# Optimization experiments

Measured on AMD Instinct MI355X. Metric: run time of the kernel, lower is better.

Reference implementation:

```python
import jax, jax.numpy as jnp
import numpy as np

H = 128  # rnn_features


def setup_inputs() -> dict:
    key = jax.random.key(0)
    ks = jax.random.split(key, 9)
    B, T, D = 1024, 256, 128
    x = jax.random.normal(ks[0], (B, T, D), dtype=jnp.float32)
    hidden_state = jax.random.normal(ks[1], (1, B, H), dtype=jnp.float32)
    done = jax.random.randint(ks[2], (B, T), 0, 2, dtype=jnp.int32)
    s = 1.0 / np.sqrt(H)
    W_ih = jax.random.uniform(ks[3], (3 * H, D), jnp.float32, -s, s)
    W_hh = jax.random.uniform(ks[4], (3 * H, H), jnp.float32, -s, s)
    b_ih = jax.random.uniform(ks[5], (3 * H,), jnp.float32, -s, s)
    b_hh = jax.random.uniform(ks[6], (3 * H,), jnp.float32, -s, s)
    fc_W = jax.random.uniform(ks[7], (H, H), jnp.float32, -s, s)
    fc_b = jax.random.uniform(ks[8], (H,), jnp.float32, -s, s)
    return {"x": x, "hidden_state": hidden_state, "done": done,
            "W_ih": W_ih, "W_hh": W_hh, "b_ih": b_ih, "b_hh": b_hh,
            "fc_W": fc_W, "fc_b": fc_b}


def _gru_with_resets(x, h0, done, W_ih, W_hh, b_ih, b_hh):
    # x: [B,T,D], h0: [B,H], done: [B,T] int
    B, T, D = x.shape
    # reset multiplier applied BEFORE step t: 1 - done[:, t-1]; no reset at t=0
    done_f = done.astype(x.dtype)
    reset = 1.0 - jnp.concatenate([jnp.zeros((B, 1), x.dtype), done_f[:, :-1]], axis=1)  # [B,T]
    # precompute input projections in one big GEMM: [B,T,3H]
    xi = jnp.einsum('btd,gd->btg', x, W_ih) + b_ih
    xi_T = jnp.transpose(xi, (1, 0, 2))      # [T,B,3H]
    reset_T = jnp.transpose(reset, (1, 0))   # [T,B]

    def step(h, inp):
        xi_t, r_t = inp
        h = h * r_t[:, None]
        gh = h @ W_hh.T + b_hh               # [B,3H]
        r = jax.nn.sigmoid(xi_t[:, :H] + gh[:, :H])
        z = jax.nn.sigmoid(xi_t[:, H:2 * H] + gh[:, H:2 * H])
        n = jnp.tanh(xi_t[:, 2 * H:] + r * gh[:, 2 * H:])
        h = (1.0 - z) * n + z * h
        return h, h

    h_last, hs = jax.lax.scan(step, h0, (xi_T, reset_T))
    return jnp.transpose(hs, (1, 0, 2)), h_last  # [B,T,H], [B,H]


def reference(x, hidden_state, done, W_ih, W_hh, b_ih, b_hh, fc_W, fc_b):
    # body_net is identity; fcs = Linear + ELU
    rfeat, h_last = _gru_with_resets(x, hidden_state[0], done, W_ih, W_hh, b_ih, b_hh)
    out = jax.nn.elu(jnp.einsum('bth,oh->bto', rfeat, fc_W) + fc_b)
    return out, h_last[None]  # hidden back to [1,B,H]
```

## Files before the change

kernel.cpp:

```cpp
#include <hip/hip_runtime.h>
#include <hip/hip_bf16.h>
#include <math.h>

#define Hd 128
#define Tt 256
#define Bb 1024
#define CL 32
#define NCK (Tt / CL)

typedef __attribute__((ext_vector_type(8))) short short8;
typedef __attribute__((ext_vector_type(4))) float f32x4;

__device__ __forceinline__ short f2bf(float f) {
    unsigned u = __float_as_uint(f);
    u += 0x7fffu + ((u >> 16) & 1u);
    return (short)(u >> 16);
}
__device__ __forceinline__ float bflo(unsigned u) { return __uint_as_float(u << 16); }
__device__ __forceinline__ float bfhi(unsigned u) { return __uint_as_float(u & 0xffff0000u); }

__global__ void prep_weights(const float* __restrict__ Wih,
                             const float* __restrict__ Whh,
                             const float* __restrict__ fcW,
                             short* __restrict__ oIh, short* __restrict__ oHh,
                             short* __restrict__ oFc) {
    int t = blockIdx.x * 256 + threadIdx.x;
    if (t >= 14336) return;
    const float* src;
    short* dst;
    if (t < 6144)       { src = Wih; dst = oIh + t * 8; }
    else if (t < 12288) { t -= 6144;  src = Whh; dst = oHh + t * 8; }
    else                { t -= 12288; src = fcW; dst = oFc + t * 8; }
    int lane = t & 63, kf = (t >> 6) & 3, nt = t >> 8;
    const float* s = src + (nt * 16 + (lane & 15)) * 128 + kf * 32 + 8 * (lane >> 4);
#pragma unroll
    for (int j = 0; j < 8; j++) dst[j] = f2bf(s[j]);
}

__global__ __launch_bounds__(512)
void xi_gemm(const float* __restrict__ x, const float* __restrict__ bih,
             const float* __restrict__ bhh, const short* __restrict__ wIh,
             short* __restrict__ xi_l) {
    __shared__ short xs[64 * 136];
    const int tid = threadIdx.x, wv = tid >> 6, ln = tid & 63;
    const int q = ln & 15, lg = ln >> 4;
    const int bg = blockIdx.x;
    const int sl0 = blockIdx.y * 4;
    {
        const int row = tid >> 3, kq = tid & 7;
        const int b = row & 15, dt = row >> 4;
        const float* xp = x + (((size_t)(bg * 16 + b)) * Tt + (sl0 + dt)) * Hd + kq * 16;
        f32x4 u0 = *(const f32x4*)&xp[0],  u1 = *(const f32x4*)&xp[4];
        f32x4 u2 = *(const f32x4*)&xp[8],  u3 = *(const f32x4*)&xp[12];
        short8 s0, s1;
#pragma unroll
        for (int i = 0; i < 4; i++) { s0[i] = f2bf(u0[i]); s0[i+4] = f2bf(u1[i]);
                                      s1[i] = f2bf(u2[i]); s1[i+4] = f2bf(u3[i]); }
        *(short8*)&xs[row * 136 + kq * 16] = s0;
        *(short8*)&xs[row * 136 + kq * 16 + 8] = s1;
    }
    __syncthreads();
    short8 wb[3][4];
#pragma unroll
    for (int i = 0; i < 3; i++)
#pragma unroll
        for (int kf = 0; kf < 4; kf++)
            wb[i][kf] = *(const short8*)&wIh[(((wv + 8 * i) * 4 + kf) * 64 + ln) * 8];
    float biasv[3];
#pragma unroll
    for (int i = 0; i < 3; i++) {
        int c = (wv + 8 * i) * 16 + q;
        biasv[i] = bih[c] + (c < 256 ? bhh[c] : 0.f);
    }
#pragma unroll 1
    for (int mt = 0; mt < 4; mt++) {
        short8 af[4];
#pragma unroll
        for (int kf = 0; kf < 4; kf++)
            af[kf] = *(const short8*)&xs[(mt * 16 + q) * 136 + kf * 32 + 8 * lg];
        f32x4 c0 = {0,0,0,0}, c1 = {0,0,0,0}, c2 = {0,0,0,0};
#pragma unroll
        for (int kf = 0; kf < 4; kf++) {
            c0 = __builtin_amdgcn_mfma_f32_16x16x32_bf16(af[kf], wb[0][kf], c0, 0, 0, 0);
            c1 = __builtin_amdgcn_mfma_f32_16x16x32_bf16(af[kf], wb[1][kf], c1, 0, 0, 0);
            c2 = __builtin_amdgcn_mfma_f32_16x16x32_bf16(af[kf], wb[2][kf], c2, 0, 0, 0);
        }
#pragma unroll
        for (int i = 0; i < 3; i++) {
            f32x4 cc = (i == 0) ? c0 : (i == 1) ? c1 : c2;
            unsigned d0 = (unsigned)(unsigned short)f2bf(cc[0] + biasv[i]) |
                          ((unsigned)(unsigned short)f2bf(cc[1] + biasv[i]) << 16);
            unsigned d1 = (unsigned)(unsigned short)f2bf(cc[2] + biasv[i]) |
                          ((unsigned)(unsigned short)f2bf(cc[3] + biasv[i]) << 16);
            uint2 dd = {d0, d1};
            ((uint2*)xi_l)[(((size_t)bg * Tt + (sl0 + mt)) * 24 + (wv + 8 * i)) * 64 + ln] = dd;
        }
    }
}

__global__ __launch_bounds__(256)
void gru_chunk(const short* __restrict__ xi_l, const int* __restrict__ done,
               const float* __restrict__ h0,
               const float* __restrict__ bhh, const float* __restrict__ fcb,
               const short* __restrict__ wHh, const short* __restrict__ wFc,
               float* __restrict__ out, float* __restrict__ hlast) {
    __shared__ short hT[2][16 * 136];
    __shared__ int doneL[Tt * 16];
    __shared__ int rbL[16];
    const int tid = threadIdx.x, j = tid >> 6, ln = tid & 63;
    const int q = ln & 15, lg = ln >> 4;
    const int bg = blockIdx.x, ck = blockIdx.y;
    const int t_c = ck * CL, t_end = t_c + CL;

    {
        const int b = tid >> 4, i = tid & 15;
        const int* dp = done + (size_t)(bg * 16 + b) * Tt;
        for (int t = i; t < t_end; t += 16) doneL[t * 16 + b] = dp[t];
    }
    __syncthreads();
    if (tid < 16) {
        int r = 0;
        for (int t = t_c - 1; t >= 0; --t)
            if (doneL[t * 16 + tid]) { r = t + 1; break; }
        rbL[tid] = r;
    }
    __syncthreads();
    int rmin = rbL[0];
#pragma unroll
    for (int b = 1; b < 16; b++) rmin = min(rmin, rbL[b]);

    short8 whh[6][4], wfc[2][4];
#pragma unroll
    for (int i = 0; i < 6; i++)
#pragma unroll
        for (int kf = 0; kf < 4; kf++)
            whh[i][kf] = *(const short8*)&wHh[(((j + 4 * i) * 4 + kf) * 64 + ln) * 8];
#pragma unroll
    for (int cs = 0; cs < 2; cs++)
#pragma unroll
        for (int kf = 0; kf < 4; kf++)
            wfc[cs][kf] = *(const short8*)&wFc[(((j + 4 * cs) * 4 + kf) * 64 + ln) * 8];
    float cbn[2], cbf[2];
#pragma unroll
    for (int cs = 0; cs < 2; cs++) {
        int c = 16 * j + 64 * cs + q;
        cbn[cs] = bhh[256 + c];
        cbf[cs] = fcb[c];
    }

    float h_reg[2][4];
#pragma unroll
    for (int cs = 0; cs < 2; cs++)
#pragma unroll
        for (int r = 0; r < 4; r++) {
            int bb = 4 * lg + r, c = 16 * j + 64 * cs + q;
            h_reg[cs][r] = (rbL[bb] == 0) ? h0[(size_t)(bg * 16 + bb) * Hd + c] : 0.f;
        }
    {
        int row = tid >> 4, c0 = (tid & 15) * 8;
        short8 s0 = {0,0,0,0,0,0,0,0};
        if (rbL[row] == 0) {
            const float* hp = &h0[(size_t)(bg * 16 + row) * Hd + c0];
            f32x4 u0 = *(const f32x4*)&hp[0], u1 = *(const f32x4*)&hp[4];
#pragma unroll
            for (int i = 0; i < 4; i++) { s0[i] = f2bf(u0[i]); s0[i+4] = f2bf(u1[i]); }
        }
        *(short8*)&hT[rmin & 1][row * 136 + c0] = s0;
    }
    __syncthreads();

    const uint2* xp = (const uint2*)xi_l + ((size_t)bg * Tt + rmin) * 1536 + j * 64 + ln;
    uint2 cur[6];
#pragma unroll
    for (int i = 0; i < 6; i++) cur[i] = xp[i * 256];
    xp += 1536;

#pragma unroll 1
    for (int t = rmin; t < t_end; ++t) {
        const short* hTp = &hT[t & 1][0];
        short* hTn = &hT[(t + 1) & 1][0];
        short8 haf[4];
#pragma unroll
        for (int kf = 0; kf < 4; kf++)
            haf[kf] = *(const short8*)&hTp[q * 136 + kf * 32 + 8 * lg];

        f32x4 acc[6];
#pragma unroll
        for (int i = 0; i < 4; i++) {
            f32x4 a = {bflo(cur[i].x), bfhi(cur[i].x), bflo(cur[i].y), bfhi(cur[i].y)};
            acc[i] = a;
        }
        { f32x4 a = {cbn[0], cbn[0], cbn[0], cbn[0]}; acc[4] = a; }
        { f32x4 a = {cbn[1], cbn[1], cbn[1], cbn[1]}; acc[5] = a; }
        uint2 xn8[2] = {cur[4], cur[5]};
        if (t + 1 < t_end) {
#pragma unroll
            for (int i = 0; i < 6; i++) cur[i] = xp[i * 256];
        }
        xp += 1536;

        if (t > t_c) {
            f32x4 fca[2];
            { f32x4 a = {cbf[0], cbf[0], cbf[0], cbf[0]}; fca[0] = a; }
            { f32x4 a = {cbf[1], cbf[1], cbf[1], cbf[1]}; fca[1] = a; }
#pragma unroll
            for (int kf = 0; kf < 4; kf++)
#pragma unroll
                for (int cs = 0; cs < 2; cs++)
                    fca[cs] = __builtin_amdgcn_mfma_f32_16x16x32_bf16(haf[kf], wfc[cs][kf], fca[cs], 0, 0, 0);
#pragma unroll
            for (int cs = 0; cs < 2; cs++)
#pragma unroll
                for (int r = 0; r < 4; r++) {
                    int bb = 4 * lg + r, c = 16 * j + 64 * cs + q;
                    float v = fca[cs][r];
                    float e = __expf(v) - 1.f;
                    v = v > 0.f ? v : e;
                    out[(((size_t)(bg * 16 + bb)) * Tt + (t - 1)) * Hd + c] = v;
                }
        }

        if (t > 0) {
            int dn = doneL[(t - 1) * 16 + q];
            short8 z8 = {0,0,0,0,0,0,0,0};
#pragma unroll
            for (int kf = 0; kf < 4; kf++) haf[kf] = dn ? z8 : haf[kf];
        }
        __builtin_amdgcn_s_setprio(1);
#pragma unroll
        for (int kf = 0; kf < 4; kf++)
#pragma unroll
            for (int i = 0; i < 6; i++)
                acc[i] = __builtin_amdgcn_mfma_f32_16x16x32_bf16(haf[kf], whh[i][kf], acc[i], 0, 0, 0);

        float rstf[4] = {1.f, 1.f, 1.f, 1.f};
        if (t > 0) {
            int4 dd = *(const int4*)&doneL[(t - 1) * 16 + 4 * lg];
            rstf[0] = dd.x ? 0.f : 1.f; rstf[1] = dd.y ? 0.f : 1.f;
            rstf[2] = dd.z ? 0.f : 1.f; rstf[3] = dd.w ? 0.f : 1.f;
        }
#pragma unroll
        for (int cs = 0; cs < 2; cs++) {
#pragma unroll
            for (int r = 0; r < 4; r++) {
                float rg = __builtin_amdgcn_rcpf(1.f + __expf(-acc[cs][r]));
                float zg = __builtin_amdgcn_rcpf(1.f + __expf(-acc[2 + cs][r]));
                float xn = (r == 0) ? bflo(xn8[cs].x) : (r == 1) ? bfhi(xn8[cs].x)
                         : (r == 2) ? bflo(xn8[cs].y) : bfhi(xn8[cs].y);
                float aa = fmaf(rg, acc[4 + cs][r], xn);
                float ng = 1.f - 2.f * __builtin_amdgcn_rcpf(__expf(2.f * aa) + 1.f);
                float hp = h_reg[cs][r] * rstf[r];
                float hn = (1.f - zg) * ng + zg * hp;
                h_reg[cs][r] = hn;
                hTn[(4 * lg + r) * 136 + 16 * j + 64 * cs + q] = f2bf(hn);
            }
        }
        __builtin_amdgcn_s_setprio(0);
        __builtin_amdgcn_sched_barrier(0);
        __builtin_amdgcn_s_waitcnt(0xC07F);
        __builtin_amdgcn_s_barrier();
        __builtin_amdgcn_sched_barrier(0);
    }
    {
        const short* hTp = &hT[t_end & 1][0];
        short8 haf[4];
#pragma unroll
        for (int kf = 0; kf < 4; kf++)
            haf[kf] = *(const short8*)&hTp[q * 136 + kf * 32 + 8 * lg];
        f32x4 fca[2];
        { f32x4 a = {cbf[0], cbf[0], cbf[0], cbf[0]}; fca[0] = a; }
        { f32x4 a = {cbf[1], cbf[1], cbf[1], cbf[1]}; fca[1] = a; }
#pragma unroll
        for (int kf = 0; kf < 4; kf++)
#pragma unroll
            for (int cs = 0; cs < 2; cs++)
                fca[cs] = __builtin_amdgcn_mfma_f32_16x16x32_bf16(haf[kf], wfc[cs][kf], fca[cs], 0, 0, 0);
#pragma unroll
        for (int cs = 0; cs < 2; cs++)
#pragma unroll
            for (int r = 0; r < 4; r++) {
                int bb = 4 * lg + r, c = 16 * j + 64 * cs + q;
                float v = fca[cs][r];
                float e = __expf(v) - 1.f;
                v = v > 0.f ? v : e;
                out[(((size_t)(bg * 16 + bb)) * Tt + (t_end - 1)) * Hd + c] = v;
            }
    }
    if (ck == NCK - 1) {
#pragma unroll
        for (int cs = 0; cs < 2; cs++)
#pragma unroll
            for (int r = 0; r < 4; r++) {
                int bb = 4 * lg + r, c = 16 * j + 64 * cs + q;
                hlast[(size_t)(bg * 16 + bb) * Hd + c] = h_reg[cs][r];
            }
    }
}

extern "C" void kernel_launch(void* const* d_in, const int* in_sizes, int n_in,
                              void* d_out, int out_size, void* d_ws, size_t ws_size,
                              hipStream_t stream) {
    const float* x   = (const float*)d_in[0];
    const float* h0  = (const float*)d_in[1];
    const int*   dn  = (const int*)d_in[2];
    const float* Wih = (const float*)d_in[3];
    const float* Whh = (const float*)d_in[4];
    const float* bih = (const float*)d_in[5];
    const float* bhh = (const float*)d_in[6];
    const float* fcW = (const float*)d_in[7];
    const float* fcb = (const float*)d_in[8];

    short* wIh = (short*)d_ws;
    short* wHh = wIh + 49152;
    short* wFc = wHh + 49152;
    short* xi_l = wFc + 16384;
    float* out = (float*)d_out;
    float* hlast = out + (size_t)Bb * Tt * Hd;

    prep_weights<<<56, 256, 0, stream>>>(Wih, Whh, fcW, wIh, wHh, wFc);
    xi_gemm<<<dim3(64, Tt / 4), 512, 0, stream>>>(x, bih, bhh, wIh, xi_l);
    gru_chunk<<<dim3(64, NCK), 256, 0, stream>>>(xi_l, dn, h0, bhh, fcb,
                                                 wHh, wFc, out, hlast);
}
```

Baseline: 164.8 us.

## Fuse input-projection GEMM into recurrent GRU kernel, dropping xi intermediate buffer

Removes the separate xi_gemm kernel and its bf16 xi intermediate buffer. The chunked GRU kernel now loads x rows per timestep, converts them to bf16 with packed cvt instructions, and computes the input projection with MFMAs inside the recurrence loop. The W_ih fragments are streamed from global/L2 each step instead of held in registers. This saves the intermediate write and read plus one launch, but adds MFMA work and weight loads to the serial per-step critical path. Chunks with a warm-up prefix also recompute the projection for the steps they replay.

```diff
diff --git a/kernel.cpp b/kernel.cpp
--- a/kernel.cpp
+++ b/kernel.cpp
@@ -16,8 +16,16 @@
     u += 0x7fffu + ((u >> 16) & 1u);
     return (short)(u >> 16);
 }
-__device__ __forceinline__ float bflo(unsigned u) { return __uint_as_float(u << 16); }
-__device__ __forceinline__ float bfhi(unsigned u) { return __uint_as_float(u & 0xffff0000u); }
+__device__ __forceinline__ f32x4 spl(float v) { f32x4 a = {v, v, v, v}; return a; }
+
+__device__ __forceinline__ short8 cvt8(f32x4 a, f32x4 b) {
+    union { unsigned u[4]; short8 s; } c;
+    asm("v_cvt_pk_bf16_f32 %0, %1, %2" : "=v"(c.u[0]) : "v"(a[0]), "v"(a[1]));
+    asm("v_cvt_pk_bf16_f32 %0, %1, %2" : "=v"(c.u[1]) : "v"(a[2]), "v"(a[3]));
+    asm("v_cvt_pk_bf16_f32 %0, %1, %2" : "=v"(c.u[2]) : "v"(b[0]), "v"(b[1]));
+    asm("v_cvt_pk_bf16_f32 %0, %1, %2" : "=v"(c.u[3]) : "v"(b[2]), "v"(b[3]));
+    return c.s;
+}
 
 __global__ void prep_weights(const float* __restrict__ Wih,
                              const float* __restrict__ Whh,
@@ -37,72 +45,21 @@
     for (int j = 0; j < 8; j++) dst[j] = f2bf(s[j]);
 }
 
-__global__ __launch_bounds__(512)
-void xi_gemm(const float* __restrict__ x, const float* __restrict__ bih,
-             const float* __restrict__ bhh, const short* __restrict__ wIh,
-             short* __restrict__ xi_l) {
-    __shared__ short xs[64 * 136];
-    const int tid = threadIdx.x, wv = tid >> 6, ln = tid & 63;
-    const int q = ln & 15, lg = ln >> 4;
-    const int bg = blockIdx.x;
-    const int sl0 = blockIdx.y * 4;
-    {
-        const int row = tid >> 3, kq = tid & 7;
-        const int b = row & 15, dt = row >> 4;
-        const float* xp = x + (((size_t)(bg * 16 + b)) * Tt + (sl0 + dt)) * Hd + kq * 16;
-        f32x4 u0 = *(const f32x4*)&xp[0],  u1 = *(const f32x4*)&xp[4];
-        f32x4 u2 = *(const f32x4*)&xp[8],  u3 = *(const f32x4*)&xp[12];
-        short8 s0, s1;
-#pragma unroll
-        for (int i = 0; i < 4; i++) { s0[i] = f2bf(u0[i]); s0[i+4] = f2bf(u1[i]);
-                                      s1[i] = f2bf(u2[i]); s1[i+4] = f2bf(u3[i]); }
-        *(short8*)&xs[row * 136 + kq * 16] = s0;
-        *(short8*)&xs[row * 136 + kq * 16 + 8] = s1;
-    }
-    __syncthreads();
-    short8 wb[3][4];
-#pragma unroll
-    for (int i = 0; i < 3; i++)
-#pragma unroll
-        for (int kf = 0; kf < 4; kf++)
-            wb[i][kf] = *(const short8*)&wIh[(((wv + 8 * i) * 4 + kf) * 64 + ln) * 8];
-    float biasv[3];
-#pragma unroll
-    for (int i = 0; i < 3; i++) {
-        int c = (wv + 8 * i) * 16 + q;
-        biasv[i] = bih[c] + (c < 256 ? bhh[c] : 0.f);
-    }
-#pragma unroll 1
-    for (int mt = 0; mt < 4; mt++) {
-        short8 af[4];
-#pragma unroll
-        for (int kf = 0; kf < 4; kf++)
-            af[kf] = *(const short8*)&xs[(mt * 16 + q) * 136 + kf * 32 + 8 * lg];
-        f32x4 c0 = {0,0,0,0}, c1 = {0,0,0,0}, c2 = {0,0,0,0};
-#pragma unroll
-        for (int kf = 0; kf < 4; kf++) {
-            c0 = __builtin_amdgcn_mfma_f32_16x16x32_bf16(af[kf], wb[0][kf], c0, 0, 0, 0);
-            c1 = __builtin_amdgcn_mfma_f32_16x16x32_bf16(af[kf], wb[1][kf], c1, 0, 0, 0);
-            c2 = __builtin_amdgcn_mfma_f32_16x16x32_bf16(af[kf], wb[2][kf], c2, 0, 0, 0);
-        }
-#pragma unroll
-        for (int i = 0; i < 3; i++) {
-            f32x4 cc = (i == 0) ? c0 : (i == 1) ? c1 : c2;
-            unsigned d0 = (unsigned)(unsigned short)f2bf(cc[0] + biasv[i]) |
-                          ((unsigned)(unsigned short)f2bf(cc[1] + biasv[i]) << 16);
-            unsigned d1 = (unsigned)(unsigned short)f2bf(cc[2] + biasv[i]) |
-                          ((unsigned)(unsigned short)f2bf(cc[3] + biasv[i]) << 16);
-            uint2 dd = {d0, d1};
-            ((uint2*)xi_l)[(((size_t)bg * Tt + (sl0 + mt)) * 24 + (wv + 8 * i)) * 64 + ln] = dd;
-        }
-    }
-}
+#define LOADW(W, i_) { const short* wb_ = wIh + ((j + 4 * (i_)) * 2048 + ln * 8); \
+    W[0] = *(const short8*)(wb_);        W[1] = *(const short8*)(wb_ + 512);      \
+    W[2] = *(const short8*)(wb_ + 1024); W[3] = *(const short8*)(wb_ + 1536); }
+#define XITILE(ACC, W) { \
+    ACC = __builtin_amdgcn_mfma_f32_16x16x32_bf16(xfrag[0], W[0], ACC, 0, 0, 0); \
+    ACC = __builtin_amdgcn_mfma_f32_16x16x32_bf16(xfrag[1], W[1], ACC, 0, 0, 0); \
+    ACC = __builtin_amdgcn_mfma_f32_16x16x32_bf16(xfrag[2], W[2], ACC, 0, 0, 0); \
+    ACC = __builtin_amdgcn_mfma_f32_16x16x32_bf16(xfrag[3], W[3], ACC, 0, 0, 0); }
 
 __global__ __launch_bounds__(256)
-void gru_chunk(const short* __restrict__ xi_l, const int* __restrict__ done,
-               const float* __restrict__ h0,
+void gru_fused(const float* __restrict__ x, const int* __restrict__ done,
+               const float* __restrict__ h0, const float* __restrict__ bih,
                const float* __restrict__ bhh, const float* __restrict__ fcb,
-               const short* __restrict__ wHh, const short* __restrict__ wFc,
+               const short* __restrict__ wIh, const short* __restrict__ wHh,
+               const short* __restrict__ wFc,
                float* __restrict__ out, float* __restrict__ hlast) {
     __shared__ short hT[2][16 * 136];
     __shared__ int doneL[Tt * 16];
@@ -140,10 +97,13 @@
 #pragma unroll
         for (int kf = 0; kf < 4; kf++)
             wfc[cs][kf] = *(const short8*)&wFc[(((j + 4 * cs) * 4 + kf) * 64 + ln) * 8];
-    float cbn[2], cbf[2];
+    float br[2], bz[2], bxn[2], cbn[2], cbf[2];
 #pragma unroll
     for (int cs = 0; cs < 2; cs++) {
         int c = 16 * j + 64 * cs + q;
+        br[cs]  = bih[c] + bhh[c];
+        bz[cs]  = bih[128 + c] + bhh[128 + c];
+        bxn[cs] = bih[256 + c];
         cbn[cs] = bhh[256 + c];
         cbf[cs] = fcb[c];
     }
@@ -169,11 +129,18 @@
     }
     __syncthreads();
 
-    const uint2* xp = (const uint2*)xi_l + ((size_t)bg * Tt + rmin) * 1536 + j * 64 + ln;
-    uint2 cur[6];
-#pragma unroll
-    for (int i = 0; i < 6; i++) cur[i] = xp[i * 256];
-    xp += 1536;
+    const float* xq = x + ((size_t)(bg * 16 + q) * Tt + rmin) * Hd + 8 * lg;
+    short8 xfrag[4];
+    {
+        f32x4 xv0[8];
+#pragma unroll
+        for (int kf = 0; kf < 4; kf++) {
+            xv0[2 * kf]     = *(const f32x4*)(xq + kf * 32);
+            xv0[2 * kf + 1] = *(const f32x4*)(xq + kf * 32 + 4);
+        }
+#pragma unroll
+        for (int kf = 0; kf < 4; kf++) xfrag[kf] = cvt8(xv0[2 * kf], xv0[2 * kf + 1]);
+    }
 
 #pragma unroll 1
     for (int t = rmin; t < t_end; ++t) {
@@ -184,25 +151,21 @@
         for (int kf = 0; kf < 4; kf++)
             haf[kf] = *(const short8*)&hTp[q * 136 + kf * 32 + 8 * lg];
 
-        f32x4 acc[6];
-#pragma unroll
-        for (int i = 0; i < 4; i++) {
-            f32x4 a = {bflo(cur[i].x), bfhi(cur[i].x), bflo(cur[i].y), bfhi(cur[i].y)};
-            acc[i] = a;
-        }
-        { f32x4 a = {cbn[0], cbn[0], cbn[0], cbn[0]}; acc[4] = a; }
-        { f32x4 a = {cbn[1], cbn[1], cbn[1], cbn[1]}; acc[5] = a; }
-        uint2 xn8[2] = {cur[4], cur[5]};
+        short8 wA[4], wB[4];
+        LOADW(wA, 0); LOADW(wB, 1);
+
+        xq += Hd;
+        f32x4 xv[8];
         if (t + 1 < t_end) {
 #pragma unroll
-            for (int i = 0; i < 6; i++) cur[i] = xp[i * 256];
-        }
-        xp += 1536;
+            for (int kf = 0; kf < 4; kf++) {
+                xv[2 * kf]     = *(const f32x4*)(xq + kf * 32);
+                xv[2 * kf + 1] = *(const f32x4*)(xq + kf * 32 + 4);
+            }
+        }
 
         if (t > t_c) {
-            f32x4 fca[2];
-            { f32x4 a = {cbf[0], cbf[0], cbf[0], cbf[0]}; fca[0] = a; }
-            { f32x4 a = {cbf[1], cbf[1], cbf[1], cbf[1]}; fca[1] = a; }
+            f32x4 fca[2] = {spl(cbf[0]), spl(cbf[1])};
 #pragma unroll
             for (int kf = 0; kf < 4; kf++)
 #pragma unroll
@@ -220,12 +183,24 @@
                 }
         }
 
+        f32x4 acc[6], axn[2];
+        acc[0] = spl(br[0]); acc[1] = spl(br[1]);
+        acc[2] = spl(bz[0]); acc[3] = spl(bz[1]);
+        axn[0] = spl(bxn[0]); axn[1] = spl(bxn[1]);
+        XITILE(acc[0], wA); LOADW(wA, 2);
+        XITILE(acc[1], wB); LOADW(wB, 3);
+        XITILE(acc[2], wA); LOADW(wA, 4);
+        XITILE(acc[3], wB); LOADW(wB, 5);
+        XITILE(axn[0], wA);
+        XITILE(axn[1], wB);
+
         if (t > 0) {
             int dn = doneL[(t - 1) * 16 + q];
             short8 z8 = {0,0,0,0,0,0,0,0};
 #pragma unroll
             for (int kf = 0; kf < 4; kf++) haf[kf] = dn ? z8 : haf[kf];
         }
+        acc[4] = spl(cbn[0]); acc[5] = spl(cbn[1]);
         __builtin_amdgcn_s_setprio(1);
 #pragma unroll
         for (int kf = 0; kf < 4; kf++)
@@ -245,8 +220,7 @@
             for (int r = 0; r < 4; r++) {
                 float rg = __builtin_amdgcn_rcpf(1.f + __expf(-acc[cs][r]));
                 float zg = __builtin_amdgcn_rcpf(1.f + __expf(-acc[2 + cs][r]));
-                float xn = (r == 0) ? bflo(xn8[cs].x) : (r == 1) ? bfhi(xn8[cs].x)
-                         : (r == 2) ? bflo(xn8[cs].y) : bfhi(xn8[cs].y);
+                float xn = axn[cs][r];
                 float aa = fmaf(rg, acc[4 + cs][r], xn);
                 float ng = 1.f - 2.f * __builtin_amdgcn_rcpf(__expf(2.f * aa) + 1.f);
                 float hp = h_reg[cs][r] * rstf[r];
@@ -256,6 +230,10 @@
             }
         }
         __builtin_amdgcn_s_setprio(0);
+        if (t + 1 < t_end) {
+#pragma unroll
+            for (int kf = 0; kf < 4; kf++) xfrag[kf] = cvt8(xv[2 * kf], xv[2 * kf + 1]);
+        }
         __builtin_amdgcn_sched_barrier(0);
         __builtin_amdgcn_s_waitcnt(0xC07F);
         __builtin_amdgcn_s_barrier();
@@ -267,9 +245,7 @@
 #pragma unroll
         for (int kf = 0; kf < 4; kf++)
             haf[kf] = *(const short8*)&hTp[q * 136 + kf * 32 + 8 * lg];
-        f32x4 fca[2];
-        { f32x4 a = {cbf[0], cbf[0], cbf[0], cbf[0]}; fca[0] = a; }
-        { f32x4 a = {cbf[1], cbf[1], cbf[1], cbf[1]}; fca[1] = a; }
+        f32x4 fca[2] = {spl(cbf[0]), spl(cbf[1])};
 #pragma unroll
         for (int kf = 0; kf < 4; kf++)
 #pragma unroll
@@ -313,12 +289,10 @@
     short* wIh = (short*)d_ws;
     short* wHh = wIh + 49152;
     short* wFc = wHh + 49152;
-    short* xi_l = wFc + 16384;
     float* out = (float*)d_out;
     float* hlast = out + (size_t)Bb * Tt * Hd;
 
     prep_weights<<<56, 256, 0, stream>>>(Wih, Whh, fcW, wIh, wHh, wFc);
-    xi_gemm<<<dim3(64, Tt / 4), 512, 0, stream>>>(x, bih, bhh, wIh, xi_l);
-    gru_chunk<<<dim3(64, NCK), 256, 0, stream>>>(xi_l, dn, h0, bhh, fcb,
-                                                 wHh, wFc, out, hlast);
-}
+    gru_fused<<<dim3(64, NCK), 256, 0, stream>>>(x, dn, h0, bih, bhh, fcb,
+                                                 wIh, wHh, wFc, out, hlast);
+}
```

Result: slower. 206.1 us (+25.1%).

## Split GRU recurrence blocks to 8 batch rows and enlarge xi_gemm tiles

Applied to the files above, without the earlier changes.

The recurrent kernel now gives each block 8 batch rows instead of 16, doubling the grid to 128x8 blocks so more CUs run the serial scan. MFMA tiles stay 16 rows wide, so half the lanes compute padding rows; their stores are masked and the padding rows of the h buffers are zeroed. The cost is wasted MFMA and gate arithmetic, and each block reloads the weight matrices. Separately, xi_gemm now handles 8 timesteps per block instead of 4, which halves its grid and reuses the loaded weight fragments across more rows.

```diff
diff --git a/kernel.cpp b/kernel.cpp
--- a/kernel.cpp
+++ b/kernel.cpp
@@ -41,23 +41,29 @@
 void xi_gemm(const float* __restrict__ x, const float* __restrict__ bih,
              const float* __restrict__ bhh, const short* __restrict__ wIh,
              short* __restrict__ xi_l) {
-    __shared__ short xs[64 * 136];
+    __shared__ short xs[128 * 136];
     const int tid = threadIdx.x, wv = tid >> 6, ln = tid & 63;
     const int q = ln & 15, lg = ln >> 4;
     const int bg = blockIdx.x;
-    const int sl0 = blockIdx.y * 4;
+    const int sl0 = blockIdx.y * 8;
     {
-        const int row = tid >> 3, kq = tid & 7;
+        const int row = tid >> 2, kq = tid & 3;
         const int b = row & 15, dt = row >> 4;
-        const float* xp = x + (((size_t)(bg * 16 + b)) * Tt + (sl0 + dt)) * Hd + kq * 16;
-        f32x4 u0 = *(const f32x4*)&xp[0],  u1 = *(const f32x4*)&xp[4];
-        f32x4 u2 = *(const f32x4*)&xp[8],  u3 = *(const f32x4*)&xp[12];
-        short8 s0, s1;
-#pragma unroll
-        for (int i = 0; i < 4; i++) { s0[i] = f2bf(u0[i]); s0[i+4] = f2bf(u1[i]);
-                                      s1[i] = f2bf(u2[i]); s1[i+4] = f2bf(u3[i]); }
-        *(short8*)&xs[row * 136 + kq * 16] = s0;
-        *(short8*)&xs[row * 136 + kq * 16 + 8] = s1;
+        const float* xp = x + (((size_t)(bg * 16 + b)) * Tt + (sl0 + dt)) * Hd + kq * 32;
+        short* dp = &xs[row * 136 + kq * 32];
+#pragma unroll
+        for (int h = 0; h < 2; h++) {
+            f32x4 u0 = *(const f32x4*)&xp[16 * h];
+            f32x4 u1 = *(const f32x4*)&xp[16 * h + 4];
+            f32x4 u2 = *(const f32x4*)&xp[16 * h + 8];
+            f32x4 u3 = *(const f32x4*)&xp[16 * h + 12];
+            short8 s0, s1;
+#pragma unroll
+            for (int i = 0; i < 4; i++) { s0[i] = f2bf(u0[i]); s0[i+4] = f2bf(u1[i]);
+                                          s1[i] = f2bf(u2[i]); s1[i+4] = f2bf(u3[i]); }
+            *(short8*)(dp + 16 * h) = s0;
+            *(short8*)(dp + 16 * h + 8) = s1;
+        }
     }
     __syncthreads();
     short8 wb[3][4];
@@ -72,8 +78,8 @@
         int c = (wv + 8 * i) * 16 + q;
         biasv[i] = bih[c] + (c < 256 ? bhh[c] : 0.f);
     }
-#pragma unroll 1
-    for (int mt = 0; mt < 4; mt++) {
+#pragma unroll 2
+    for (int mt = 0; mt < 8; mt++) {
         short8 af[4];
 #pragma unroll
         for (int kf = 0; kf < 4; kf++)
@@ -105,29 +111,30 @@
                const short* __restrict__ wHh, const short* __restrict__ wFc,
                float* __restrict__ out, float* __restrict__ hlast) {
     __shared__ short hT[2][16 * 136];
-    __shared__ int doneL[Tt * 16];
-    __shared__ int rbL[16];
+    __shared__ int doneL[Tt * 8];
+    __shared__ int rbL[8];
     const int tid = threadIdx.x, j = tid >> 6, ln = tid & 63;
     const int q = ln & 15, lg = ln >> 4;
-    const int bg = blockIdx.x, ck = blockIdx.y;
+    const int gb = blockIdx.x, ck = blockIdx.y;
+    const int g16 = gb >> 1, h = gb & 1;
     const int t_c = ck * CL, t_end = t_c + CL;
 
     {
-        const int b = tid >> 4, i = tid & 15;
-        const int* dp = done + (size_t)(bg * 16 + b) * Tt;
-        for (int t = i; t < t_end; t += 16) doneL[t * 16 + b] = dp[t];
+        const int b = tid >> 5, i = tid & 31;
+        const int* dp = done + (size_t)(gb * 8 + b) * Tt;
+        for (int t = i; t < t_end; t += 32) doneL[t * 8 + b] = dp[t];
     }
     __syncthreads();
-    if (tid < 16) {
+    if (tid < 8) {
         int r = 0;
         for (int t = t_c - 1; t >= 0; --t)
-            if (doneL[t * 16 + tid]) { r = t + 1; break; }
+            if (doneL[t * 8 + tid]) { r = t + 1; break; }
         rbL[tid] = r;
     }
     __syncthreads();
     int rmin = rbL[0];
 #pragma unroll
-    for (int b = 1; b < 16; b++) rmin = min(rmin, rbL[b]);
+    for (int b = 1; b < 8; b++) rmin = min(rmin, rbL[b]);
 
     short8 whh[6][4], wfc[2][4];
 #pragma unroll
@@ -148,28 +155,33 @@
         cbf[cs] = fcb[c];
     }
 
+    const bool act = (lg < 2);
     float h_reg[2][4];
 #pragma unroll
     for (int cs = 0; cs < 2; cs++)
 #pragma unroll
         for (int r = 0; r < 4; r++) {
-            int bb = 4 * lg + r, c = 16 * j + 64 * cs + q;
-            h_reg[cs][r] = (rbL[bb] == 0) ? h0[(size_t)(bg * 16 + bb) * Hd + c] : 0.f;
+            int bb = (4 * lg + r) & 7, c = 16 * j + 64 * cs + q;
+            h_reg[cs][r] = (act && rbL[bb] == 0)
+                               ? h0[(size_t)(gb * 8 + bb) * Hd + c] : 0.f;
         }
     {
         int row = tid >> 4, c0 = (tid & 15) * 8;
-        short8 s0 = {0,0,0,0,0,0,0,0};
-        if (rbL[row] == 0) {
-            const float* hp = &h0[(size_t)(bg * 16 + row) * Hd + c0];
+        short8 z8 = {0,0,0,0,0,0,0,0};
+        short8 s0 = z8;
+        if (row < 8 && rbL[row] == 0) {
+            const float* hp = &h0[(size_t)(gb * 8 + row) * Hd + c0];
             f32x4 u0 = *(const f32x4*)&hp[0], u1 = *(const f32x4*)&hp[4];
 #pragma unroll
             for (int i = 0; i < 4; i++) { s0[i] = f2bf(u0[i]); s0[i+4] = f2bf(u1[i]); }
         }
+        *(short8*)&hT[(rmin & 1) ^ 1][row * 136 + c0] = z8;
         *(short8*)&hT[rmin & 1][row * 136 + c0] = s0;
     }
     __syncthreads();
 
-    const uint2* xp = (const uint2*)xi_l + ((size_t)bg * Tt + rmin) * 1536 + j * 64 + ln;
+    const int lnx = (2 * h + (lg & 1)) * 16 + q;
+    const uint2* xp = (const uint2*)xi_l + ((size_t)g16 * Tt + rmin) * 1536 + j * 64 + lnx;
     uint2 cur[6];
 #pragma unroll
     for (int i = 0; i < 6; i++) cur[i] = xp[i * 256];
@@ -208,20 +220,22 @@
 #pragma unroll
                 for (int cs = 0; cs < 2; cs++)
                     fca[cs] = __builtin_amdgcn_mfma_f32_16x16x32_bf16(haf[kf], wfc[cs][kf], fca[cs], 0, 0, 0);
-#pragma unroll
-            for (int cs = 0; cs < 2; cs++)
-#pragma unroll
-                for (int r = 0; r < 4; r++) {
-                    int bb = 4 * lg + r, c = 16 * j + 64 * cs + q;
-                    float v = fca[cs][r];
-                    float e = __expf(v) - 1.f;
-                    v = v > 0.f ? v : e;
-                    out[(((size_t)(bg * 16 + bb)) * Tt + (t - 1)) * Hd + c] = v;
-                }
+            if (act) {
+#pragma unroll
+                for (int cs = 0; cs < 2; cs++)
+#pragma unroll
+                    for (int r = 0; r < 4; r++) {
+                        int bb = 4 * lg + r, c = 16 * j + 64 * cs + q;
+                        float v = fca[cs][r];
+                        float e = __expf(v) - 1.f;
+                        v = v > 0.f ? v : e;
+                        out[(((size_t)(gb * 8 + bb)) * Tt + (t - 1)) * Hd + c] = v;
+                    }
+            }
         }
 
         if (t > 0) {
-            int dn = doneL[(t - 1) * 16 + q];
+            int dn = doneL[(t - 1) * 8 + (q & 7)];
             short8 z8 = {0,0,0,0,0,0,0,0};
 #pragma unroll
             for (int kf = 0; kf < 4; kf++) haf[kf] = dn ? z8 : haf[kf];
@@ -235,7 +249,7 @@
 
         float rstf[4] = {1.f, 1.f, 1.f, 1.f};
         if (t > 0) {
-            int4 dd = *(const int4*)&doneL[(t - 1) * 16 + 4 * lg];
+            int4 dd = *(const int4*)&doneL[(t - 1) * 8 + ((4 * lg) & 7)];
             rstf[0] = dd.x ? 0.f : 1.f; rstf[1] = dd.y ? 0.f : 1.f;
             rstf[2] = dd.z ? 0.f : 1.f; rstf[3] = dd.w ? 0.f : 1.f;
         }
@@ -252,7 +266,8 @@
                 float hp = h_reg[cs][r] * rstf[r];
                 float hn = (1.f - zg) * ng + zg * hp;
                 h_reg[cs][r] = hn;
-                hTn[(4 * lg + r) * 136 + 16 * j + 64 * cs + q] = f2bf(hn);
+                if (act)
+                    hTn[(4 * lg + r) * 136 + 16 * j + 64 * cs + q] = f2bf(hn);
             }
         }
         __builtin_amdgcn_s_setprio(0);
@@ -275,24 +290,26 @@
 #pragma unroll
             for (int cs = 0; cs < 2; cs++)
                 fca[cs] = __builtin_amdgcn_mfma_f32_16x16x32_bf16(haf[kf], wfc[cs][kf], fca[cs], 0, 0, 0);
+        if (act) {
+#pragma unroll
+            for (int cs = 0; cs < 2; cs++)
+#pragma unroll
+                for (int r = 0; r < 4; r++) {
+                    int bb = 4 * lg + r, c = 16 * j + 64 * cs + q;
+                    float v = fca[cs][r];
+                    float e = __expf(v) - 1.f;
+                    v = v > 0.f ? v : e;
+                    out[(((size_t)(gb * 8 + bb)) * Tt + (t_end - 1)) * Hd + c] = v;
+                }
+        }
+    }
+    if (ck == NCK - 1 && act) {
 #pragma unroll
         for (int cs = 0; cs < 2; cs++)
 #pragma unroll
             for (int r = 0; r < 4; r++) {
                 int bb = 4 * lg + r, c = 16 * j + 64 * cs + q;
-                float v = fca[cs][r];
-                float e = __expf(v) - 1.f;
-                v = v > 0.f ? v : e;
-                out[(((size_t)(bg * 16 + bb)) * Tt + (t_end - 1)) * Hd + c] = v;
-            }
-    }
-    if (ck == NCK - 1) {
-#pragma unroll
-        for (int cs = 0; cs < 2; cs++)
-#pragma unroll
-            for (int r = 0; r < 4; r++) {
-                int bb = 4 * lg + r, c = 16 * j + 64 * cs + q;
-                hlast[(size_t)(bg * 16 + bb) * Hd + c] = h_reg[cs][r];
+                hlast[(size_t)(gb * 8 + bb) * Hd + c] = h_reg[cs][r];
             }
     }
 }
@@ -318,7 +335,7 @@
     float* hlast = out + (size_t)Bb * Tt * Hd;
 
     prep_weights<<<56, 256, 0, stream>>>(Wih, Whh, fcW, wIh, wHh, wFc);
-    xi_gemm<<<dim3(64, Tt / 4), 512, 0, stream>>>(x, bih, bhh, wIh, xi_l);
-    gru_chunk<<<dim3(64, NCK), 256, 0, stream>>>(xi_l, dn, h0, bhh, fcb,
-                                                 wHh, wFc, out, hlast);
-}
+    xi_gemm<<<dim3(64, Tt / 8), 512, 0, stream>>>(x, bih, bhh, wIh, xi_l);
+    gru_chunk<<<dim3(128, NCK), 256, 0, stream>>>(xi_l, dn, h0, bhh, fcb,
+                                                  wHh, wFc, out, hlast);
+}
```

Result: slower. 223.8 us (+35.8%).
